# Kernel tuning notes

Hardware: AMD Instinct MI355X
Metric: run time of the kernel (lower is better)

The kernel has to match this reference:

```python
import jax, jax.numpy as jnp
import numpy as np

_COUNTS = [256, 192, 128, 64]


def _l2norm(x, axis=1):
    # F.normalize(p=2): x / max(||x||, eps)
    return x / jnp.maximum(jnp.linalg.norm(x, axis=axis, keepdims=True), 1e-12)


def _gcn(x, w1, b1, w2, b2, w3, b3):
    # stack of kernel-size-1 Conv1d == channel matmuls; x: [B, C, N]
    h = jax.nn.relu(jnp.einsum('oc,bcn->bon', w1, x) + b1[:, None])
    h = jax.nn.relu(jnp.einsum('oc,bcn->bon', w2, h) + b2[:, None])
    return jnp.einsum('oc,bcn->bon', w3, h) + b3[:, None]


def setup_inputs() -> dict:
    key = jax.random.key(0)
    ks = iter(jax.random.split(key, 64))
    feat_shapes = [(8, 256, 100, 100), (8, 512, 50, 50), (8, 1024, 25, 25), (8, 2048, 13, 13)]
    chans = [256, 512, 1024, 2048]
    C = 256
    d = {}
    for i, s in enumerate(feat_shapes):
        d[f'feat{i}'] = jax.random.normal(next(ks), s, jnp.float32)
    for i, (ci, ni) in enumerate(zip(chans, _COUNTS)):
        d[f'w_sem_{i}'] = jax.random.normal(next(ks), (ni, ci), jnp.float32) * 0.02
        d[f'w_emb_{i}'] = jax.random.normal(next(ks), (C, ci), jnp.float32) * 0.02
        d[f'w_q_{i}'] = jax.random.normal(next(ks), (C, ci), jnp.float32) * 0.02
        d[f'w_out_{i}'] = jax.random.normal(next(ks), (C, C), jnp.float32) * 0.02
        d[f'w_res_{i}'] = jax.random.normal(next(ks), (C, ci), jnp.float32) * 0.02
    d['gw1'] = jax.random.normal(next(ks), (4, 64, C), jnp.float32) * 0.05
    d['gb1'] = jnp.zeros((4, 64), jnp.float32)
    d['gw2'] = jax.random.normal(next(ks), (4, 64, 64), jnp.float32) * 0.05
    d['gb2'] = jnp.zeros((4, 64), jnp.float32)
    d['gw3'] = jax.random.normal(next(ks), (4, C, 64), jnp.float32) * 0.05
    d['gb3'] = jnp.zeros((4, C), jnp.float32)
    d['mw1'] = jax.random.normal(next(ks), (64, C), jnp.float32) * 0.05
    d['mb1'] = jnp.zeros((64,), jnp.float32)
    d['mw2'] = jax.random.normal(next(ks), (64, 64), jnp.float32) * 0.05
    d['mb2'] = jnp.zeros((64,), jnp.float32)
    d['mw3'] = jax.random.normal(next(ks), (C, 64), jnp.float32) * 0.05
    d['mb3'] = jnp.zeros((C,), jnp.float32)
    return d


def reference(feat0, feat1, feat2, feat3,
              w_sem_0, w_sem_1, w_sem_2, w_sem_3,
              w_emb_0, w_emb_1, w_emb_2, w_emb_3,
              w_q_0, w_q_1, w_q_2, w_q_3,
              w_out_0, w_out_1, w_out_2, w_out_3,
              w_res_0, w_res_1, w_res_2, w_res_3,
              gw1, gb1, gw2, gb2, gw3, gb3,
              mw1, mb1, mw2, mb2, mw3, mb3):
    feats = [feat0, feat1, feat2, feat3]
    w_sem = [w_sem_0, w_sem_1, w_sem_2, w_sem_3]
    w_emb = [w_emb_0, w_emb_1, w_emb_2, w_emb_3]
    w_q = [w_q_0, w_q_1, w_q_2, w_q_3]
    w_out = [w_out_0, w_out_1, w_out_2, w_out_3]
    w_res = [w_res_0, w_res_1, w_res_2, w_res_3]

    # ---- context collector ----
    contexts = []
    for i in range(4):
        f = feats[i]
        B, ci, H, W = f.shape
        hw = H * W
        sem = jnp.einsum('nc,bchw->bnhw', w_sem[i], f)                 # [B, ni, H, W]
        emb = jnp.einsum('oc,bchw->bohw', w_emb[i], f).reshape(B, -1, hw)  # [B, C, HW]
        fn = _l2norm(f, 1).reshape(B, ci, hw)
        en = _l2norm(sem, 1).reshape(B, -1, hw)
        # torch.einsum('bni,bci->bni') sums over c -> entities * sum_c(features)
        sim = en * fn.sum(axis=1, keepdims=True) * jnp.sqrt(jnp.float32(ci))
        attn = jax.nn.softmax(sim, axis=2)                              # softmax over HW
        contexts.append(jnp.einsum('bop,bnp->bon', emb, attn))          # [B, C, ni]

    # ---- graph reasoning ----
    refined = [_gcn(c, gw1[i], gb1[i], gw2[i], gb2[i], gw3[i], gb3[i]) + c
               for i, c in enumerate(contexts)]
    g = jnp.concatenate(refined, axis=2)                                # [B, C, 640]
    g = _gcn(g, mw1, mb1, mw2, mb2, mw3, mb3) + g

    # ---- context distributor ----
    outs = []
    ptr = 0
    for i in range(4):
        f = feats[i]
        B, ci, H, W = f.shape
        hw = H * W
        ni = _COUNTS[i]
        lc = g[:, :, ptr:ptr + ni]                                      # [B, C, ni]
        ptr += ni
        q = jnp.einsum('oc,bchw->bohw', w_q[i], f).reshape(B, -1, hw)   # [B, C, HW]
        scores = jnp.einsum('bop,bon->bpn', _l2norm(q, 1), _l2norm(lc, 1))  # [B, HW, ni]
        aw = jax.nn.softmax(scores, axis=2)                             # softmax over ni
        wc = jnp.einsum('bon,bpn->bop', lc, aw).reshape(B, -1, H, W)    # [B, C, H, W]
        out = jnp.einsum('oc,bchw->bohw', w_out[i], wc) + jnp.einsum('oc,bchw->bohw', w_res[i], f)
        outs.append(out)
    return tuple(outs)
```

## Files before the change

kernel.cpp:

```cpp
#include <hip/hip_runtime.h>
#include <math.h>


#define BB 8
#define CC 256
#define GG 640

typedef __attribute__((ext_vector_type(8))) short short8;
typedef __attribute__((ext_vector_type(4))) float f32x4;

__device__ __forceinline__ unsigned short f2bf(float f) {
    unsigned int u = __float_as_uint(f);
    u += 0x7fffu + ((u >> 16) & 1u);
    return (unsigned short)(u >> 16);
}
__device__ __forceinline__ float bf2f(unsigned short h) {
    return __uint_as_float(((unsigned int)h) << 16);
}
__device__ __forceinline__ float h2f(unsigned short h) {
    union { unsigned short u; _Float16 x; } cv; cv.u = h; return (float)cv.x;
}
__device__ __forceinline__ unsigned short f2h(float f) {
    union { unsigned short u; _Float16 x; } cv; cv.x = (_Float16)f; return cv.u;
}

__device__ __forceinline__ void glds16(const unsigned short* g, unsigned short* l) {
    __builtin_amdgcn_global_load_lds(
        (const __attribute__((address_space(1))) void*)g,
        (__attribute__((address_space(3))) void*)l, 16, 0, 0);
}

__global__ __launch_bounds__(256) void mfmaGemm(
    const unsigned short* __restrict__ A, long sA, int lda,
    const unsigned short* __restrict__ B, long sB, int ldb,
    void* __restrict__ C, long sC, int ldc, long offC,
    int M, int N, int K, int kChunks, int kChunkLen, int mode,
    int gxn, int gym,
    void* __restrict__ C2, long sC2, int ldc2, long offC2, int M1, int mode2)
{
    __shared__ __align__(16) unsigned short As[2][128 * 32];
    __shared__ __align__(16) unsigned short Bs[2][128 * 32];

    const int nb = (int)gridDim.x;
    int orig = (int)blockIdx.x;
    int xcd = orig & 7, idx = orig >> 3;
    int q8 = nb >> 3, r8 = nb & 7;
    int wg = (xcd < r8) ? (xcd * (q8 + 1) + idx)
                        : (r8 * (q8 + 1) + (xcd - r8) * q8 + idx);
    int mb, nbk, z;
    if (N >= M) { mb = wg % gym; int t = wg / gym; nbk = t % gxn; z = t / gxn; }
    else        { nbk = wg % gxn; int t = wg / gxn; mb = t % gym; z = t / gym; }

    const int b = z / kChunks, chunk = z - b * kChunks;
    const int kbeg = chunk * kChunkLen;
    const int kend = min(K, kbeg + kChunkLen);
    const int m0 = mb * 128, n0 = nbk * 128;

    const unsigned short* Ab = A + (long)b * sA;
    const unsigned short* Bb = B + (long)b * sB;

    const int tid = threadIdx.x;
    const int row = tid >> 2, seg = tid & 3;
    const int wave = tid >> 6, lane = tid & 63;
    const int wm = (wave & 1) * 64, wn = (wave >> 1) * 64;
    const int lm = lane & 15, kq = lane >> 4;

    const bool okA = ((lda & 7) == 0) && ((((size_t)Ab) & 15) == 0);
    const bool okB = ((ldb & 7) == 0) && ((((size_t)Bb) & 15) == 0);

    f32x4 acc[4][4];
    #pragma unroll
    for (int i = 0; i < 4; ++i)
        #pragma unroll
        for (int j = 0; j < 4; ++j) acc[i][j] = (f32x4){0.f, 0.f, 0.f, 0.f};

    auto stageF = [&](const unsigned short* Pb, int ld, int o0,
                      unsigned short* LS, int kg) {
        #pragma unroll
        for (int l = 0; l < 2; ++l) {
            const unsigned short* src = Pb + (long)(o0 + l * 64 + row) * ld + kg + seg * 8;
            glds16(src, &LS[(l * 64 + row) * 32 + seg * 8]);
        }
    };
    auto stageS = [&](const unsigned short* Pb, int ld, int lim, int o0,
                      unsigned short* LS, int kg) {
        int kgg = kg + seg * 8;
        int krem = kend - kgg;
        #pragma unroll
        for (int l = 0; l < 2; ++l) {
            int g = o0 + l * 64 + row;
            uint4 v = make_uint4(0u, 0u, 0u, 0u);
            if (g < lim && krem > 0) {
                const unsigned short* src = Pb + (long)g * ld + kgg;
                if (krem >= 8 && ((((size_t)src) & 15) == 0)) {
                    v = *(const uint4*)src;
                } else {
                    __align__(16) unsigned short tmp[8] = {0,0,0,0,0,0,0,0};
                    int c = krem < 8 ? krem : 8;
                    for (int j = 0; j < c; ++j) tmp[j] = src[j];
                    v = *(const uint4*)tmp;
                }
            }
            *(uint4*)&LS[(l * 64 + row) * 32 + seg * 8] = v;
        }
    };
    auto stage = [&](int kg, int buf) {
        bool full = (kg + 32 <= kend);
        if (okA && full) stageF(Ab, lda, m0, As[buf], kg);
        else             stageS(Ab, lda, M, m0, As[buf], kg);
        if (okB && full) stageF(Bb, ldb, n0, Bs[buf], kg);
        else             stageS(Bb, ldb, N, n0, Bs[buf], kg);
    };

    stage(kbeg, 0);
    int cur = 0;
    for (int k0 = kbeg; k0 < kend; k0 += 32) {
        __syncthreads();
        if (k0 + 32 < kend) stage(k0 + 32, cur ^ 1);

        short8 af[4], bfr[4];
        #pragma unroll
        for (int mt = 0; mt < 4; ++mt)
            af[mt] = *(const short8*)&As[cur][(wm + mt * 16 + lm) * 32 + kq * 8];
        #pragma unroll
        for (int nt = 0; nt < 4; ++nt)
            bfr[nt] = *(const short8*)&Bs[cur][(wn + nt * 16 + lm) * 32 + kq * 8];
        #pragma unroll
        for (int mt = 0; mt < 4; ++mt)
            #pragma unroll
            for (int nt = 0; nt < 4; ++nt)
                acc[mt][nt] = __builtin_amdgcn_mfma_f32_16x16x32_bf16(
                    af[mt], bfr[nt], acc[mt][nt], 0, 0, 0);
        cur ^= 1;
    }

    const long cb1 = (long)b * sC + offC;
    const long cb2 = (long)b * sC2 + offC2;
    #pragma unroll
    for (int mt = 0; mt < 4; ++mt) {
        #pragma unroll
        for (int nt = 0; nt < 4; ++nt) {
            int n_g = n0 + wn + nt * 16 + lm;
            if (n_g >= N) continue;
            #pragma unroll
            for (int r = 0; r < 4; ++r) {
                int m_g = m0 + wm + mt * 16 + kq * 4 + r;
                if (m_g >= M) continue;
                float v = acc[mt][nt][r];
                void* Cp; int md; long cix;
                if (m_g < M1) { Cp = C;  md = mode;  cix = cb1 + (long)m_g * ldc + n_g; }
                else          { Cp = C2; md = mode2; cix = cb2 + (long)(m_g - M1) * ldc2 + n_g; }
                if (md == 0)      ((float*)Cp)[cix] = v;
                else if (md == 1) ((float*)Cp)[cix] += v;
                else if (md == 2) atomicAdd(&((float*)Cp)[cix], v);
                else if (md == 3) ((unsigned short*)Cp)[cix] = f2h(v);
                else              ((unsigned short*)Cp)[cix] = f2bf(v);
            }
        }
    }
}

__global__ __launch_bounds__(256) void gemmA(
    const float* __restrict__ W, long sW,
    const float* __restrict__ X, long sX, int ldx, long offX,
    float* __restrict__ Cd, long sC, int ldc, long offC,
    const float* __restrict__ bias,
    const float* __restrict__ res, long sR, int ldr, long offR,
    int O, int K, int P, int relu, int accum,
    int lvlFuse, long wStride, int bStride)
{
    __shared__ float Ws[16][64];
    __shared__ float Xs[16][64];
    const int tid = threadIdx.x;
    const int tx = tid & 15;
    const int ty = tid >> 4;
    const int b  = blockIdx.z;
    const int o0 = blockIdx.y * 64;
    const int p0 = blockIdx.x * 64;

    const float* Wp = W;
    const float* bp = bias;
    if (lvlFuse) {
        int lvl = p0 >= 576 ? 3 : p0 >= 448 ? 2 : p0 >= 256 ? 1 : 0;
        Wp += (long)lvl * wStride;
        if (bias) bp += (long)lvl * bStride;
    }
    const float* Wb = Wp + (long)b * sW;
    const float* Xb = X + (long)b * sX + offX;

    float acc[4][4] = {};

    const int wo = tid >> 2;
    const int wk = (tid & 3) * 4;
    const int xp = tid & 63;
    const int xq = tid >> 6;

    for (int k0 = 0; k0 < K; k0 += 16) {
        #pragma unroll
        for (int u = 0; u < 4; ++u) {
            int kk = wk + u;
            float v = 0.f;
            if (o0 + wo < O && k0 + kk < K) v = Wb[(long)(o0 + wo) * K + k0 + kk];
            Ws[kk][wo] = v;
        }
        #pragma unroll
        for (int u = 0; u < 4; ++u) {
            int kk = xq * 4 + u;
            float v = 0.f;
            if (p0 + xp < P && k0 + kk < K) v = Xb[(long)(k0 + kk) * ldx + (p0 + xp)];
            Xs[kk][xp] = v;
        }
        __syncthreads();
        #pragma unroll
        for (int kk = 0; kk < 16; ++kk) {
            float4 wv = *(const float4*)&Ws[kk][ty * 4];
            float4 xv = *(const float4*)&Xs[kk][tx * 4];
            float wa[4] = {wv.x, wv.y, wv.z, wv.w};
            float xa[4] = {xv.x, xv.y, xv.z, xv.w};
            #pragma unroll
            for (int i = 0; i < 4; ++i)
                #pragma unroll
                for (int j = 0; j < 4; ++j)
                    acc[i][j] += wa[i] * xa[j];
        }
        __syncthreads();
    }

    #pragma unroll
    for (int i = 0; i < 4; ++i) {
        int o = o0 + ty * 4 + i;
        if (o >= O) continue;
        #pragma unroll
        for (int j = 0; j < 4; ++j) {
            int p = p0 + tx * 4 + j;
            if (p >= P) continue;
            float v = acc[i][j];
            if (bias) v += bp[o];
            if (relu) v = fmaxf(v, 0.f);
            if (res)  v += res[(long)b * sR + offR + (long)o * ldr + p];
            long ci_ = (long)b * sC + offC + (long)o * ldc + p;
            if (accum) Cd[ci_] += v; else Cd[ci_] = v;
        }
    }
}

__global__ __launch_bounds__(256) void transCvtF(
    const float* __restrict__ src, long sS, int R, int Cc,
    unsigned short* __restrict__ dst, long sD,
    const float* __restrict__ scale, long sScale)
{
    __shared__ float tile[32][33];
    int b = blockIdx.z;
    int r0 = blockIdx.y * 32, c0 = blockIdx.x * 32;
    const float* sb = src + (long)b * sS;
    unsigned short* db = dst + (long)b * sD;
    int tr = threadIdx.x >> 5, tc = threadIdx.x & 31;
    #pragma unroll
    for (int it = 0; it < 4; ++it) {
        int r = r0 + tr + it * 8, c = c0 + tc;
        tile[tr + it * 8][tc] = (r < R && c < Cc) ? sb[(long)r * Cc + c] : 0.f;
    }
    __syncthreads();
    #pragma unroll
    for (int it = 0; it < 4; ++it) {
        int c = c0 + tr + it * 8;
        int r = r0 + tc;
        if (c < Cc && r < R) {
            float v = tile[tc][tr + it * 8];
            if (scale) v *= scale[(long)b * sScale + c];
            db[(long)c * R + r] = f2bf(v);
        }
    }
}

__global__ __launch_bounds__(256) void transCvtH(
    const unsigned short* __restrict__ src, long sS, int R, int Cc,
    unsigned short* __restrict__ dst, long sD,
    const float* __restrict__ scale, long sScale)
{
    __shared__ float tile[32][33];
    int b = blockIdx.z;
    int r0 = blockIdx.y * 32, c0 = blockIdx.x * 32;
    const unsigned short* sb = src + (long)b * sS;
    unsigned short* db = dst + (long)b * sD;
    int tr = threadIdx.x >> 5, tc = threadIdx.x & 31;
    #pragma unroll
    for (int it = 0; it < 4; ++it) {
        int r = r0 + tr + it * 8, c = c0 + tc;
        tile[tr + it * 8][tc] = (r < R && c < Cc) ? h2f(sb[(long)r * Cc + c]) : 0.f;
    }
    __syncthreads();
    #pragma unroll
    for (int it = 0; it < 4; ++it) {
        int c = c0 + tr + it * 8;
        int r = r0 + tc;
        if (c < Cc && r < R) {
            float v = tile[tc][tr + it * 8];
            if (scale) v *= scale[(long)b * sScale + c];
            db[(long)c * R + r] = f2bf(v);
        }
    }
}

__global__ __launch_bounds__(256) void posStatsT(
    const unsigned short* __restrict__ featT, float* __restrict__ fscale,
    int ci, int hw, float sq)
{
    int b = blockIdx.y, p = blockIdx.x;
    const unsigned short* row = featT + ((long)b * hw + p) * ci;
    float s = 0.f, ss = 0.f;
    for (int c = threadIdx.x; c < ci; c += 256) {
        float v = bf2f(row[c]); s += v; ss += v * v;
    }
    __shared__ float rs[256], rss[256];
    int tid = threadIdx.x;
    rs[tid] = s; rss[tid] = ss; __syncthreads();
    for (int st = 128; st > 0; st >>= 1) {
        if (tid < st) { rs[tid] += rs[tid + st]; rss[tid] += rss[tid + st]; }
        __syncthreads();
    }
    if (tid == 0)
        fscale[(long)b * hw + p] = rs[0] / fmaxf(sqrtf(rss[0]), 1e-12f) * sq;
}

__global__ void enScale(const unsigned short* __restrict__ sem, float* __restrict__ fscale,
                        int ni, int hw)
{
    int b = blockIdx.y;
    int p = blockIdx.x * 256 + threadIdx.x;
    if (p >= hw) return;
    const unsigned short* sb = sem + (long)b * ni * hw + p;
    float ss = 0.f;
    for (int n = 0; n < ni; ++n) { float v = h2f(sb[(long)n * hw]); ss += v * v; }
    fscale[(long)b * hw + p] = fscale[(long)b * hw + p] / fmaxf(sqrtf(ss), 1e-12f);
}

__global__ __launch_bounds__(256) void softmaxHW(
    unsigned short* buf, const float* __restrict__ scale, int ni, int hw)
{
    int b = blockIdx.y, n = blockIdx.x;
    unsigned short* row = buf + ((long)b * ni + n) * hw;
    const float* sc = scale + (long)b * hw;
    __shared__ float red[256];
    int tid = threadIdx.x;

    float m = -1e30f;
    for (int p = tid; p < hw; p += 256) m = fmaxf(m, h2f(row[p]) * sc[p]);
    red[tid] = m; __syncthreads();
    for (int s = 128; s > 0; s >>= 1) {
        if (tid < s) red[tid] = fmaxf(red[tid], red[tid + s]);
        __syncthreads();
    }
    m = red[0]; __syncthreads();

    float sum = 0.f;
    for (int p = tid; p < hw; p += 256) sum += __expf(h2f(row[p]) * sc[p] - m);
    red[tid] = sum; __syncthreads();
    for (int s = 128; s > 0; s >>= 1) {
        if (tid < s) red[tid] += red[tid + s];
        __syncthreads();
    }
    float inv = 1.0f / red[0];

    for (int p = tid; p < hw; p += 256) {
        float v = __expf(h2f(row[p]) * sc[p] - m) * inv;
        row[p] = f2bf(v);
    }
}

__global__ void softmaxN(unsigned short* buf, int hw, int ni)
{
    int b = blockIdx.y;
    int wav = threadIdx.x >> 6, lane = threadIdx.x & 63;
    int p = blockIdx.x * 4 + wav;
    if (p >= hw) return;
    unsigned short* row = buf + ((long)b * hw + p) * ni;
    float m = -1e30f;
    for (int n = lane; n < ni; n += 64) m = fmaxf(m, h2f(row[n]));
    for (int off = 32; off > 0; off >>= 1) m = fmaxf(m, __shfl_xor(m, off));
    float s = 0.f;
    for (int n = lane; n < ni; n += 64) s += __expf(h2f(row[n]) - m);
    for (int off = 32; off > 0; off >>= 1) s += __shfl_xor(s, off);
    float inv = 1.f / s;
    for (int n = lane; n < ni; n += 64) {
        float v = __expf(h2f(row[n]) - m) * inv;
        row[n] = f2bf(v);
    }
}

__global__ void lcRnorm(const float* __restrict__ g2, float* __restrict__ lcr)
{
    int b = blockIdx.y;
    int col = blockIdx.x * 256 + threadIdx.x;
    if (col >= GG) return;
    const float* gb = g2 + (long)b * CC * GG + col;
    float ss = 0.f;
    for (int o = 0; o < CC; ++o) { float v = gb[o * GG]; ss += v * v; }
    lcr[b * GG + col] = 1.f / fmaxf(sqrtf(ss), 1e-12f);
}

__global__ void buildLc(const float* __restrict__ g2, const float* __restrict__ lcr,
                        unsigned short* __restrict__ lcnT, unsigned short* __restrict__ lcB,
                        int ni, int ptr)
{
    long t = (long)blockIdx.x * 256 + threadIdx.x;
    if (t >= (long)BB * ni * CC) return;
    int o = (int)(t & (CC - 1));
    long r = t >> 8;
    int n = (int)(r % ni);
    int b = (int)(r / ni);
    float raw = g2[(long)b * CC * GG + (long)o * GG + ptr + n];
    lcnT[t] = f2bf(raw * lcr[b * GG + ptr + n]);
    lcB[((long)b * CC + o) * ni + n] = f2bf(raw);
}

__global__ void qNormCol(const unsigned short* __restrict__ q, float* __restrict__ scl, int hw)
{
    int b = blockIdx.y;
    int p = blockIdx.x * 256 + threadIdx.x;
    if (p >= hw) return;
    const unsigned short* qb = q + (long)b * CC * hw + p;
    float ss = 0.f;
    for (int o = 0; o < CC; ++o) { float v = h2f(qb[(long)o * hw]); ss += v * v; }
    scl[(long)b * hw + p] = 1.f / fmaxf(sqrtf(ss), 1e-12f);
}

struct CvtJob { const float* src; long off; int n; int pad; };
struct CvtJobs { CvtJob j[20]; };
__global__ void cvtAllK(CvtJobs jobs, unsigned short* __restrict__ dst)
{
    const CvtJob J = jobs.j[blockIdx.y];
    int t = blockIdx.x * 256 + threadIdx.x;
    if (t < J.n) dst[J.off + t] = f2bf(J.src[t]);
}

__global__ void cvtOut(const float* __restrict__ src, unsigned short* __restrict__ dst,
                       int n, int toF16)
{
    int i = blockIdx.x * 256 + threadIdx.x;
    if (i >= n) return;
    float v = src[i];
    dst[i] = toF16 ? f2h(v) : f2bf(v);
}

extern "C" void kernel_launch(void* const* d_in, const int* in_sizes, int n_in,
                              void* d_out, int out_size, void* d_ws, size_t ws_size,
                              hipStream_t stream)
{
    (void)n_in; (void)out_size;
    static const int  CI[4]  = {256, 512, 1024, 2048};
    static const int  NI[4]  = {256, 192, 128, 64};
    static const int  HWs[4] = {10000, 2500, 625, 169};
    static const int  PTR[4] = {0, 256, 448, 576};
    static const long OUTOFF[4] = {0, 20480000L, 25600000L, 26880000L};

    const float* feat[4];
    for (int i = 0; i < 4; ++i) feat[i] = (const float*)d_in[i];

    const float *w_sem[4], *w_emb[4], *w_q[4], *w_out[4], *w_res[4];
    bool grouped = (in_sizes[5] == 192 * 512);
    for (int i = 0; i < 4; ++i) {
        if (grouped) {
            w_sem[i] = (const float*)d_in[4 + i];
            w_emb[i] = (const float*)d_in[8 + i];
            w_q[i]   = (const float*)d_in[12 + i];
            w_out[i] = (const float*)d_in[16 + i];
            w_res[i] = (const float*)d_in[20 + i];
        } else {
            int base = 4 + 5 * i;
            w_sem[i] = (const float*)d_in[base + 0];
            w_emb[i] = (const float*)d_in[base + 1];
            w_q[i]   = (const float*)d_in[base + 2];
            w_out[i] = (const float*)d_in[base + 3];
            w_res[i] = (const float*)d_in[base + 4];
        }
    }
    const float* gw1 = (const float*)d_in[24];
    const float* gb1 = (const float*)d_in[25];
    const float* gw2 = (const float*)d_in[26];
    const float* gb2 = (const float*)d_in[27];
    const float* gw3 = (const float*)d_in[28];
    const float* gb3 = (const float*)d_in[29];
    const float* mw1 = (const float*)d_in[30];
    const float* mb1 = (const float*)d_in[31];
    const float* mw2 = (const float*)d_in[32];
    const float* mb2 = (const float*)d_in[33];
    const float* mw3 = (const float*)d_in[34];
    const float* mb3 = (const float*)d_in[35];

    char* wp = (char*)d_ws;
    auto carve = [&](size_t bytes) { char* r = wp; wp += (bytes + 255) & ~(size_t)255; return r; };
    unsigned short* R1 = (unsigned short*)carve(40960000);
    unsigned short* R2 = (unsigned short*)carve(40960000);
    unsigned short* R3 = (unsigned short*)carve(40960000);
    float* ctxg = (float*)carve(5242880);
    float* gbuf = (float*)carve(5242880);
    float* g2   = (float*)carve(5242880);
    float* h1   = (float*)carve(1310720);
    float* h2   = (float*)carve(1310720);
    unsigned short* lcnT = (unsigned short*)carve(1048576);
    unsigned short* lcB  = (unsigned short*)carve(1048576);
    float* lcr  = (float*)carve(20480);
    float* scl  = (float*)carve(320000);
    float* SK   = (float*)carve(5120000);
    unsigned short* wbuf = (unsigned short*)carve(7275520);

    unsigned short* featP[4];
    featP[0] = R1;
    {
        size_t f1 = 2UL * BB * 2500 * 512;
        size_t f2 = 2UL * BB * 625 * 1024;
        size_t f3 = 2UL * BB * 169 * 2048;
        size_t used = (size_t)(wp - (char*)d_ws);
        bool persist = (used + f1 + f2 + f3 + (1u << 20) + 4096) <= ws_size;
        if (persist) {
            featP[1] = (unsigned short*)carve(f1);
            featP[2] = (unsigned short*)carve(f2);
            featP[3] = (unsigned short*)carve(f3);
            carve(1u << 20);
        } else {
            featP[1] = featP[2] = featP[3] = R1;
        }
    }
    bool persist = (featP[1] != R1);

    float* outp = (float*)d_out;

    CvtJobs jobs;
    unsigned short *wsemB[4], *wembB[4], *wqB[4], *woutB[4], *wresB[4];
    long woff = 0; int maxn = 0, jx = 0;
    auto addJob = [&](const float* s, int n, unsigned short** outp_) {
        jobs.j[jx].src = s; jobs.j[jx].off = woff; jobs.j[jx].n = n; jobs.j[jx].pad = 0;
        *outp_ = wbuf + woff;
        woff += (n + 7) & ~7;
        if (n > maxn) maxn = n;
        ++jx;
    };
    for (int i = 0; i < 4; ++i) {
        addJob(w_sem[i], NI[i] * CI[i], &wsemB[i]);
        addJob(w_emb[i], CC * CI[i],    &wembB[i]);
        addJob(w_q[i],   CC * CI[i],    &wqB[i]);
        addJob(w_res[i], CC * CI[i],    &wresB[i]);
        addJob(w_out[i], CC * CC,       &woutB[i]);
    }
    cvtAllK<<<dim3((maxn + 255) / 256, 20), 256, 0, stream>>>(jobs, wbuf);

    auto mgSeg = [&](const unsigned short* A, long sA, int lda,
                     const unsigned short* Bp, long sB, int ldb,
                     void* Cp, long sC, int ldc, long offC,
                     int M, int N, int K, int mode, int kc,
                     void* C2, long sC2, int ldc2, long offC2, int M1, int mode2) {
        if (kc < 1) kc = 1;
        int kLen = ((K + kc - 1) / kc + 31) & ~31;
        int kcc = (K + kLen - 1) / kLen;
        int gxn = (N + 127) / 128, gym = (M + 127) / 128;
        dim3 g((unsigned)(gxn * gym * BB * kcc));
        mfmaGemm<<<g, 256, 0, stream>>>(A, sA, lda, Bp, sB, ldb,
                                        Cp, sC, ldc, offC, M, N, K, kcc, kLen, mode,
                                        gxn, gym, C2, sC2, ldc2, offC2, M1, mode2);
    };
    auto mg = [&](const unsigned short* A, long sA, int lda,
                  const unsigned short* Bp, long sB, int ldb,
                  void* Cp, long sC, int ldc, long offC,
                  int M, int N, int K, int mode, int kc) {
        mgSeg(A, sA, lda, Bp, sB, ldb, Cp, sC, ldc, offC, M, N, K, mode, kc,
              nullptr, 0, 1, 0, M, 0);
    };
    auto projTo = [&](const unsigned short* Wbf, int K, const unsigned short* Xt, long sXt,
                      unsigned short* dst, int M, int N, int fmode) {
        int blocks = ((M + 127) / 128) * ((N + 127) / 128) * BB;
        if (blocks >= 256 || K < 512) {
            mg(Wbf, 0, K, Xt, sXt, K, dst, (long)M * N, N, 0, M, N, K, fmode, 1);
        } else {
            int kc = (256 + blocks - 1) / blocks;
            hipMemsetAsync(SK, 0, (size_t)BB * M * N * 4, stream);
            mg(Wbf, 0, K, Xt, sXt, K, SK, (long)M * N, N, 0, M, N, K, 2, kc);
            long tot = (long)BB * M * N;
            cvtOut<<<dim3((unsigned)((tot + 255) / 256)), 256, 0, stream>>>(
                SK, dst, (int)tot, fmode == 3 ? 1 : 0);
        }
    };

    hipMemsetAsync(ctxg, 0, (size_t)BB * CC * GG * 4, stream);

    for (int i = 0; i < 4; ++i) {
        int ci = CI[i], ni = NI[i], hw = HWs[i];
        unsigned short* fT = featP[i];
        transCvtF<<<dim3((hw + 31) / 32, (ci + 31) / 32, BB), 256, 0, stream>>>(
            feat[i], (long)ci * hw, ci, hw, fT, (long)hw * ci, nullptr, 0);
        posStatsT<<<dim3(hw, BB), 256, 0, stream>>>(fT, scl, ci, hw, sqrtf((float)ci));
        if (i < 2) {
            mgSeg(wsemB[i], 0, ci, fT, (long)hw * ci, ci,
                  R2, (long)ni * hw, hw, 0,
                  ni + CC, hw, ci, 3, 1,
                  R3, (long)CC * hw, hw, 0, ni, 4);
        } else {
            projTo(wsemB[i], ci, fT, (long)hw * ci, R2, ni, hw, 3);
            projTo(wembB[i], ci, fT, (long)hw * ci, R3, CC, hw, 4);
        }
        enScale<<<dim3((hw + 255) / 256, BB), 256, 0, stream>>>(R2, scl, ni, hw);
        softmaxHW<<<dim3(ni, BB), 256, 0, stream>>>(R2, scl, ni, hw);
        {
            int blocks = ((CC + 127) / 128) * ((ni + 127) / 128) * BB;
            int kc = (blocks < 256 && hw >= 512) ? (256 + blocks - 1) / blocks : 1;
            mg(R3, (long)CC * hw, hw, R2, (long)ni * hw, hw,
               ctxg, (long)CC * GG, GG, PTR[i], CC, ni, hw, 2, kc);
        }
    }

    {
        dim3 gl(GG / 64, 1, BB);
        gemmA<<<gl, 256, 0, stream>>>(gw1, 0, ctxg, (long)CC * GG, GG, 0,
                                      h1, (long)64 * GG, GG, 0, gb1,
                                      nullptr, 0, 0, 0, 64, CC, GG, 1, 0,
                                      1, (long)64 * CC, 64);
        gemmA<<<gl, 256, 0, stream>>>(gw2, 0, h1, (long)64 * GG, GG, 0,
                                      h2, (long)64 * GG, GG, 0, gb2,
                                      nullptr, 0, 0, 0, 64, 64, GG, 1, 0,
                                      1, (long)64 * 64, 64);
        dim3 gl2(GG / 64, CC / 64, BB);
        gemmA<<<gl2, 256, 0, stream>>>(gw3, 0, h2, (long)64 * GG, GG, 0,
                                       gbuf, (long)CC * GG, GG, 0, gb3,
                                       ctxg, (long)CC * GG, GG, 0, CC, 64, GG, 0, 0,
                                       1, (long)CC * 64, CC);
    }
    {
        dim3 gl(GG / 64, 1, BB);
        gemmA<<<gl, 256, 0, stream>>>(mw1, 0, gbuf, (long)CC * GG, GG, 0,
                                      h1, (long)64 * GG, GG, 0, mb1,
                                      nullptr, 0, 0, 0, 64, CC, GG, 1, 0, 0, 0, 0);
        gemmA<<<gl, 256, 0, stream>>>(mw2, 0, h1, (long)64 * GG, GG, 0,
                                      h2, (long)64 * GG, GG, 0, mb2,
                                      nullptr, 0, 0, 0, 64, 64, GG, 1, 0, 0, 0, 0);
        dim3 gl2(GG / 64, CC / 64, BB);
        gemmA<<<gl2, 256, 0, stream>>>(mw3, 0, h2, (long)64 * GG, GG, 0,
                                       g2, (long)CC * GG, GG, 0, mb3,
                                       gbuf, (long)CC * GG, GG, 0, CC, 64, GG, 0, 0, 0, 0, 0);
    }

    lcRnorm<<<dim3(3, BB), 256, 0, stream>>>(g2, lcr);

    for (int i = 0; i < 4; ++i) {
        int ci = CI[i], ni = NI[i], hw = HWs[i];
        long tot = (long)BB * ni * CC;
        buildLc<<<dim3((unsigned)((tot + 255) / 256)), 256, 0, stream>>>(
            g2, lcr, lcnT, lcB, ni, PTR[i]);
        unsigned short* fT = featP[i];
        if (!persist)
            transCvtF<<<dim3((hw + 31) / 32, (ci + 31) / 32, BB), 256, 0, stream>>>(
                feat[i], (long)ci * hw, ci, hw, fT, (long)hw * ci, nullptr, 0);
        if (i < 2) {
            mgSeg(wqB[i], 0, ci, fT, (long)hw * ci, ci,
                  R2, (long)CC * hw, hw, 0,
                  2 * CC, hw, ci, 3, 1,
                  outp, (long)CC * hw, hw, OUTOFF[i], CC, 0);
        } else {
            projTo(wqB[i], ci, fT, (long)hw * ci, R2, CC, hw, 3);
        }
        qNormCol<<<dim3((hw + 255) / 256, BB), 256, 0, stream>>>(R2, scl, hw);
        transCvtH<<<dim3((hw + 31) / 32, (CC + 31) / 32, BB), 256, 0, stream>>>(
            R2, (long)CC * hw, CC, hw, R3, (long)hw * CC, scl, hw);
        mg(R3, (long)hw * CC, CC, lcnT, (long)ni * CC, CC,
           R2, (long)hw * ni, ni, 0, hw, ni, CC, 3, 1);
        softmaxN<<<dim3((hw + 3) / 4, BB), 256, 0, stream>>>(R2, hw, ni);
        mg(R2, (long)hw * ni, ni, lcB, (long)CC * ni, ni,
           R3, (long)hw * CC, CC, 0, hw, CC, ni, 4, 1);
        if (i >= 2) {
            int blocks = ((CC + 127) / 128) * ((hw + 127) / 128) * BB;
            if (blocks >= 256 || ci < 512) {
                mg(wresB[i], 0, ci, fT, (long)hw * ci, ci,
                   outp, (long)CC * hw, hw, OUTOFF[i], CC, hw, ci, 0, 1);
            } else {
                int kc = (256 + blocks - 1) / blocks;
                hipMemsetAsync(outp + OUTOFF[i], 0, (size_t)BB * CC * hw * 4, stream);
                mg(wresB[i], 0, ci, fT, (long)hw * ci, ci,
                   outp, (long)CC * hw, hw, OUTOFF[i], CC, hw, ci, 2, kc);
            }
        }
        mg(woutB[i], 0, CC, R3, (long)hw * CC, CC,
           outp, (long)CC * hw, hw, OUTOFF[i], CC, hw, CC, 1, 1);
    }
}
```

Before: 2.127 ms.

## Fuse output and residual projections into one concatenated-K GEMM, swizzle LDS

Packs w_out and w_res into a single [C, C+ci] bf16 weight so the output and residual projections become one GEMM whose B operand switches from the wc buffer to the feature buffer at K=C. This removes a separate accumulate pass over the output and the q/res split path for the first two levels. It also adds an XOR swizzle to the LDS tile layout to reduce bank conflicts on MFMA fragment loads. The cost is extra branching in the staging code and a larger K for the fused GEMM.

```diff
diff --git a/kernel.cpp b/kernel.cpp
--- a/kernel.cpp
+++ b/kernel.cpp
@@ -30,9 +30,12 @@
         (__attribute__((address_space(3))) void*)l, 16, 0, 0);
 }
 
+__device__ __forceinline__ int swz(int row, int seg) { return seg ^ ((row >> 1) & 3); }
+
 __global__ __launch_bounds__(256) void mfmaGemm(
     const unsigned short* __restrict__ A, long sA, int lda,
     const unsigned short* __restrict__ B, long sB, int ldb,
+    const unsigned short* __restrict__ B2p, long sB2, int ldb2, int Kb,
     void* __restrict__ C, long sC, int ldc, long offC,
     int M, int N, int K, int kChunks, int kChunkLen, int mode,
     int gxn, int gym,
@@ -56,8 +59,9 @@
     const int kend = min(K, kbeg + kChunkLen);
     const int m0 = mb * 128, n0 = nbk * 128;
 
-    const unsigned short* Ab = A + (long)b * sA;
-    const unsigned short* Bb = B + (long)b * sB;
+    const unsigned short* Ab  = A + (long)b * sA;
+    const unsigned short* Bb  = B + (long)b * sB;
+    const unsigned short* Bb2 = B2p ? (B2p + (long)b * sB2) : nullptr;
 
     const int tid = threadIdx.x;
     const int row = tid >> 2, seg = tid & 3;
@@ -65,8 +69,9 @@
     const int wm = (wave & 1) * 64, wn = (wave >> 1) * 64;
     const int lm = lane & 15, kq = lane >> 4;
 
-    const bool okA = ((lda & 7) == 0) && ((((size_t)Ab) & 15) == 0);
-    const bool okB = ((ldb & 7) == 0) && ((((size_t)Bb) & 15) == 0);
+    const bool okA  = ((lda  & 7) == 0) && ((((size_t)Ab)  & 15) == 0);
+    const bool okB  = ((ldb  & 7) == 0) && ((((size_t)Bb)  & 15) == 0);
+    const bool okB2 = Bb2 && ((ldb2 & 7) == 0) && ((((size_t)Bb2) & 15) == 0);
 
     f32x4 acc[4][4];
     #pragma unroll
@@ -78,17 +83,19 @@
                       unsigned short* LS, int kg) {
         #pragma unroll
         for (int l = 0; l < 2; ++l) {
-            const unsigned short* src = Pb + (long)(o0 + l * 64 + row) * ld + kg + seg * 8;
-            glds16(src, &LS[(l * 64 + row) * 32 + seg * 8]);
+            int rf = l * 64 + row;
+            const unsigned short* src = Pb + (long)(o0 + rf) * ld + kg + swz(rf, seg) * 8;
+            glds16(src, &LS[rf * 32 + seg * 8]);
         }
     };
     auto stageS = [&](const unsigned short* Pb, int ld, int lim, int o0,
-                      unsigned short* LS, int kg) {
-        int kgg = kg + seg * 8;
-        int krem = kend - kgg;
+                      unsigned short* LS, int kg, int lend) {
         #pragma unroll
         for (int l = 0; l < 2; ++l) {
-            int g = o0 + l * 64 + row;
+            int rf = l * 64 + row;
+            int kgg = kg + swz(rf, seg) * 8;
+            int krem = lend - kgg;
+            int g = o0 + rf;
             uint4 v = make_uint4(0u, 0u, 0u, 0u);
             if (g < lim && krem > 0) {
                 const unsigned short* src = Pb + (long)g * ld + kgg;
@@ -101,15 +108,21 @@
                     v = *(const uint4*)tmp;
                 }
             }
-            *(uint4*)&LS[(l * 64 + row) * 32 + seg * 8] = v;
+            *(uint4*)&LS[rf * 32 + seg * 8] = v;
         }
     };
     auto stage = [&](int kg, int buf) {
         bool full = (kg + 32 <= kend);
         if (okA && full) stageF(Ab, lda, m0, As[buf], kg);
-        else             stageS(Ab, lda, M, m0, As[buf], kg);
-        if (okB && full) stageF(Bb, ldb, n0, Bs[buf], kg);
-        else             stageS(Bb, ldb, N, n0, Bs[buf], kg);
+        else             stageS(Ab, lda, M, m0, As[buf], kg, kend);
+        if (kg < Kb) {
+            if (okB && full) stageF(Bb, ldb, n0, Bs[buf], kg);
+            else             stageS(Bb, ldb, N, n0, Bs[buf], kg, min(kend, Kb));
+        } else {
+            int kl = kg - Kb;
+            if (okB2 && full) stageF(Bb2, ldb2, n0, Bs[buf], kl);
+            else              stageS(Bb2, ldb2, N, n0, Bs[buf], kl, kend - Kb);
+        }
     };
 
     stage(kbeg, 0);
@@ -120,11 +133,15 @@
 
         short8 af[4], bfr[4];
         #pragma unroll
-        for (int mt = 0; mt < 4; ++mt)
-            af[mt] = *(const short8*)&As[cur][(wm + mt * 16 + lm) * 32 + kq * 8];
-        #pragma unroll
-        for (int nt = 0; nt < 4; ++nt)
-            bfr[nt] = *(const short8*)&Bs[cur][(wn + nt * 16 + lm) * 32 + kq * 8];
+        for (int mt = 0; mt < 4; ++mt) {
+            int rA = wm + mt * 16 + lm;
+            af[mt] = *(const short8*)&As[cur][rA * 32 + swz(rA, kq) * 8];
+        }
+        #pragma unroll
+        for (int nt = 0; nt < 4; ++nt) {
+            int rB = wn + nt * 16 + lm;
+            bfr[nt] = *(const short8*)&Bs[cur][rB * 32 + swz(rB, kq) * 8];
+        }
         #pragma unroll
         for (int mt = 0; mt < 4; ++mt)
             #pragma unroll
@@ -425,13 +442,16 @@
     scl[(long)b * hw + p] = 1.f / fmaxf(sqrtf(ss), 1e-12f);
 }
 
-struct CvtJob { const float* src; long off; int n; int pad; };
+struct CvtJob { const float* src; long off; int n; int K; int ld; int colOff; };
 struct CvtJobs { CvtJob j[20]; };
 __global__ void cvtAllK(CvtJobs jobs, unsigned short* __restrict__ dst)
 {
     const CvtJob J = jobs.j[blockIdx.y];
     int t = blockIdx.x * 256 + threadIdx.x;
-    if (t < J.n) dst[J.off + t] = f2bf(J.src[t]);
+    if (t < J.n) {
+        int r = t / J.K, c = t - r * J.K;
+        dst[J.off + (long)r * J.ld + J.colOff + c] = f2bf(J.src[t]);
+    }
 }
 
 __global__ void cvtOut(const float* __restrict__ src, unsigned short* __restrict__ dst,
@@ -503,7 +523,7 @@
     float* lcr  = (float*)carve(20480);
     float* scl  = (float*)carve(320000);
     float* SK   = (float*)carve(5120000);
-    unsigned short* wbuf = (unsigned short*)carve(7275520);
+    unsigned short* wbuf = (unsigned short*)carve(7500000);
 
     unsigned short* featP[4];
     featP[0] = R1;
@@ -512,8 +532,8 @@
         size_t f2 = 2UL * BB * 625 * 1024;
         size_t f3 = 2UL * BB * 169 * 2048;
         size_t used = (size_t)(wp - (char*)d_ws);
-        bool persist = (used + f1 + f2 + f3 + (1u << 20) + 4096) <= ws_size;
-        if (persist) {
+        bool ok = (used + f1 + f2 + f3 + (1u << 20) + 4096) <= ws_size;
+        if (ok) {
             featP[1] = (unsigned short*)carve(f1);
             featP[2] = (unsigned short*)carve(f2);
             featP[3] = (unsigned short*)carve(f3);
@@ -527,35 +547,42 @@
     float* outp = (float*)d_out;
 
     CvtJobs jobs;
-    unsigned short *wsemB[4], *wembB[4], *wqB[4], *woutB[4], *wresB[4];
+    unsigned short *wsemB[4], *wqB[4], *woutresB[4];
     long woff = 0; int maxn = 0, jx = 0;
-    auto addJob = [&](const float* s, int n, unsigned short** outp_) {
-        jobs.j[jx].src = s; jobs.j[jx].off = woff; jobs.j[jx].n = n; jobs.j[jx].pad = 0;
-        *outp_ = wbuf + woff;
-        woff += (n + 7) & ~7;
+    auto addJob = [&](const float* s, int n, int K, int ld, int colOff, long off) {
+        jobs.j[jx].src = s; jobs.j[jx].off = off; jobs.j[jx].n = n;
+        jobs.j[jx].K = K; jobs.j[jx].ld = ld; jobs.j[jx].colOff = colOff;
         if (n > maxn) maxn = n;
         ++jx;
     };
     for (int i = 0; i < 4; ++i) {
-        addJob(w_sem[i], NI[i] * CI[i], &wsemB[i]);
-        addJob(w_emb[i], CC * CI[i],    &wembB[i]);
-        addJob(w_q[i],   CC * CI[i],    &wqB[i]);
-        addJob(w_res[i], CC * CI[i],    &wresB[i]);
-        addJob(w_out[i], CC * CC,       &woutB[i]);
-    }
+        int ci = CI[i], ni = NI[i];
+        wsemB[i] = wbuf + woff;
+        addJob(w_sem[i], ni * ci, ci, ci, 0, woff);  woff += ni * ci;
+        addJob(w_emb[i], CC * ci, ci, ci, 0, woff);  woff += CC * ci;
+        wqB[i] = wbuf + woff;
+        addJob(w_q[i],   CC * ci, ci, ci, 0, woff);  woff += CC * ci;
+        woutresB[i] = wbuf + woff;
+        addJob(w_out[i], CC * CC, CC, CC + ci, 0,  woff);
+        addJob(w_res[i], CC * ci, ci, CC + ci, CC, woff);
+        woff += (long)CC * (CC + ci);
+    }
+
     cvtAllK<<<dim3((maxn + 255) / 256, 20), 256, 0, stream>>>(jobs, wbuf);
 
-    auto mgSeg = [&](const unsigned short* A, long sA, int lda,
-                     const unsigned short* Bp, long sB, int ldb,
-                     void* Cp, long sC, int ldc, long offC,
-                     int M, int N, int K, int mode, int kc,
-                     void* C2, long sC2, int ldc2, long offC2, int M1, int mode2) {
+    auto mgFull = [&](const unsigned short* A, long sA, int lda,
+                      const unsigned short* B1, long sB1, int ldb1,
+                      const unsigned short* B2, long sB2, int ldb2, int Kb,
+                      void* Cp, long sC, int ldc, long offC,
+                      int M, int N, int K, int mode, int kc,
+                      void* C2, long sC2, int ldc2, long offC2, int M1, int mode2) {
         if (kc < 1) kc = 1;
         int kLen = ((K + kc - 1) / kc + 31) & ~31;
         int kcc = (K + kLen - 1) / kLen;
         int gxn = (N + 127) / 128, gym = (M + 127) / 128;
         dim3 g((unsigned)(gxn * gym * BB * kcc));
-        mfmaGemm<<<g, 256, 0, stream>>>(A, sA, lda, Bp, sB, ldb,
+        mfmaGemm<<<g, 256, 0, stream>>>(A, sA, lda, B1, sB1, ldb1,
+                                        B2, sB2, ldb2, Kb,
                                         Cp, sC, ldc, offC, M, N, K, kcc, kLen, mode,
                                         gxn, gym, C2, sC2, ldc2, offC2, M1, mode2);
     };
@@ -563,8 +590,9 @@
                   const unsigned short* Bp, long sB, int ldb,
                   void* Cp, long sC, int ldc, long offC,
                   int M, int N, int K, int mode, int kc) {
-        mgSeg(A, sA, lda, Bp, sB, ldb, Cp, sC, ldc, offC, M, N, K, mode, kc,
-              nullptr, 0, 1, 0, M, 0);
+        mgFull(A, sA, lda, Bp, sB, ldb, nullptr, 0, 8, K,
+               Cp, sC, ldc, offC, M, N, K, mode, kc,
+               nullptr, 0, 1, 0, M, 0);
     };
     auto projTo = [&](const unsigned short* Wbf, int K, const unsigned short* Xt, long sXt,
                       unsigned short* dst, int M, int N, int fmode) {
@@ -590,13 +618,13 @@
             feat[i], (long)ci * hw, ci, hw, fT, (long)hw * ci, nullptr, 0);
         posStatsT<<<dim3(hw, BB), 256, 0, stream>>>(fT, scl, ci, hw, sqrtf((float)ci));
         if (i < 2) {
-            mgSeg(wsemB[i], 0, ci, fT, (long)hw * ci, ci,
-                  R2, (long)ni * hw, hw, 0,
-                  ni + CC, hw, ci, 3, 1,
-                  R3, (long)CC * hw, hw, 0, ni, 4);
+            mgFull(wsemB[i], 0, ci, fT, (long)hw * ci, ci, nullptr, 0, 8, ci,
+                   R2, (long)ni * hw, hw, 0,
+                   ni + CC, hw, ci, 3, 1,
+                   R3, (long)CC * hw, hw, 0, ni, 4);
         } else {
             projTo(wsemB[i], ci, fT, (long)hw * ci, R2, ni, hw, 3);
-            projTo(wembB[i], ci, fT, (long)hw * ci, R3, CC, hw, 4);
+            projTo(wsemB[i] + (long)ni * ci, ci, fT, (long)hw * ci, R3, CC, hw, 4);
         }
         enScale<<<dim3((hw + 255) / 256, BB), 256, 0, stream>>>(R2, scl, ni, hw);
         softmaxHW<<<dim3(ni, BB), 256, 0, stream>>>(R2, scl, ni, hw);
@@ -649,14 +677,7 @@
         if (!persist)
             transCvtF<<<dim3((hw + 31) / 32, (ci + 31) / 32, BB), 256, 0, stream>>>(
                 feat[i], (long)ci * hw, ci, hw, fT, (long)hw * ci, nullptr, 0);
-        if (i < 2) {
-            mgSeg(wqB[i], 0, ci, fT, (long)hw * ci, ci,
-                  R2, (long)CC * hw, hw, 0,
-                  2 * CC, hw, ci, 3, 1,
-                  outp, (long)CC * hw, hw, OUTOFF[i], CC, 0);
-        } else {
-            projTo(wqB[i], ci, fT, (long)hw * ci, R2, CC, hw, 3);
-        }
+        projTo(wqB[i], ci, fT, (long)hw * ci, R2, CC, hw, 3);
         qNormCol<<<dim3((hw + 255) / 256, BB), 256, 0, stream>>>(R2, scl, hw);
         transCvtH<<<dim3((hw + 31) / 32, (CC + 31) / 32, BB), 256, 0, stream>>>(
             R2, (long)CC * hw, CC, hw, R3, (long)hw * CC, scl, hw);
@@ -665,19 +686,22 @@
         softmaxN<<<dim3((hw + 3) / 4, BB), 256, 0, stream>>>(R2, hw, ni);
         mg(R2, (long)hw * ni, ni, lcB, (long)CC * ni, ni,
            R3, (long)hw * CC, CC, 0, hw, CC, ni, 4, 1);
-        if (i >= 2) {
+        {
+            int K = CC + ci;
             int blocks = ((CC + 127) / 128) * ((hw + 127) / 128) * BB;
-            if (blocks >= 256 || ci < 512) {
-                mg(wresB[i], 0, ci, fT, (long)hw * ci, ci,
-                   outp, (long)CC * hw, hw, OUTOFF[i], CC, hw, ci, 0, 1);
+            if (blocks >= 256) {
+                mgFull(woutresB[i], 0, K, R3, (long)hw * CC, CC,
+                       fT, (long)hw * ci, ci, CC,
+                       outp, (long)CC * hw, hw, OUTOFF[i], CC, hw, K, 0, 1,
+                       nullptr, 0, 1, 0, CC, 0);
             } else {
                 int kc = (256 + blocks - 1) / blocks;
                 hipMemsetAsync(outp + OUTOFF[i], 0, (size_t)BB * CC * hw * 4, stream);
-                mg(wresB[i], 0, ci, fT, (long)hw * ci, ci,
-                   outp, (long)CC * hw, hw, OUTOFF[i], CC, hw, ci, 2, kc);
+                mgFull(woutresB[i], 0, K, R3, (long)hw * CC, CC,
+                       fT, (long)hw * ci, ci, CC,
+                       outp, (long)CC * hw, hw, OUTOFF[i], CC, hw, K, 2, kc,
+                       nullptr, 0, 1, 0, CC, 0);
             }
         }
-        mg(woutB[i], 0, CC, R3, (long)hw * CC, CC,
-           outp, (long)CC * hw, hw, OUTOFF[i], CC, hw, CC, 1, 1);
-    }
-}
+    }
+}
```

Measured after the change: 1.984 ms. 1.07x faster.
